# Performance work log

Hardware: AMD Instinct MI355X
Metric: run time of the kernel (lower is better)

The kernel has to match this reference:

```python
import jax, jax.numpy as jnp
import numpy as np
import math

BATCH, SEQ, D_MODEL, D_STATE = 8, 512, 2048, 16
DT_MIN, DT_MAX, DT_FLOOR, DT_SCALE = 0.001, 0.1, 1e-4, 1.0


def setup_inputs() -> dict:
    key = jax.random.key(0)
    k1, k2, k3, k4, k5 = jax.random.split(key, 5)
    x = jax.random.normal(k1, (BATCH, SEQ, D_MODEL), dtype=jnp.float32)
    # A_log = -exp(randn / sqrt(d_state))  (so A = exp(A_log) in (0,1))
    A_log = -jnp.exp(jax.random.normal(k2, (D_MODEL, D_STATE), dtype=jnp.float32) / math.sqrt(D_STATE))
    B = jax.random.normal(k3, (D_MODEL, D_STATE), dtype=jnp.float32) / math.sqrt(D_STATE)
    C = jax.random.normal(k4, (D_MODEL, D_STATE), dtype=jnp.float32) / math.sqrt(D_STATE)
    log_dt = jax.random.uniform(k5, (D_MODEL,), dtype=jnp.float32) * (math.log(DT_MAX) - math.log(DT_MIN)) + math.log(DT_MIN)
    log_dt = jnp.maximum(log_dt, jnp.float32(math.log(DT_FLOOR)))
    return {"x": x, "A_log": A_log, "B": B, "C": C, "log_dt": log_dt}


def reference(x, A_log, B, C, log_dt):
    # delta=None path: dt is per-channel, time-invariant -> dA, dB are [D, N]
    dt = jnp.exp(log_dt) * DT_SCALE                      # [D]
    A = jnp.exp(A_log)                                   # [D, N]
    dA = jnp.exp(dt[:, None] * A)                        # [D, N]  (matches torch einsum 'bld,dn->bldn' squeezed)
    dB = dt[:, None] * B                                 # [D, N]
    batch = x.shape[0]
    h0 = jnp.zeros((batch, D_MODEL, D_STATE), dtype=x.dtype)

    def step(h, xt):
        # xt: [B, D]
        h = dA * h + dB * xt[:, :, None]                 # [B, D, N]
        y = jnp.einsum('bdn,dn->bd', h, C)               # [B, D]
        return h, y

    _, ys = jax.lax.scan(step, h0, jnp.swapaxes(x, 0, 1))  # ys: [L, B, D]
    return jnp.swapaxes(ys, 0, 1)                          # [B, L, D]
```

## Files before the change

kernel.cpp:

```cpp
#include <hip/hip_runtime.h>
#include <math.h>


#define SSM_BATCH 8
#define SSM_SEQ 512
#define SSM_D 2048
#define SSM_N 16
#define NC 16
#define CL 32
#define DPB 64

typedef float float4v __attribute__((ext_vector_type(4)));

static __device__ inline float4v fma4(float4v a, float4v b, float4v c) {
    return (float4v){fmaf(a.x, b.x, c.x), fmaf(a.y, b.y, c.y),
                     fmaf(a.z, b.z, c.z), fmaf(a.w, b.w, c.w)};
}
static __device__ inline float4v exp4(float4v v) {
    return (float4v){expf(v.x), expf(v.y), expf(v.z), expf(v.w)};
}

__global__ __launch_bounds__(1024, 4) void ssm_fused3(
    const float* __restrict__ x, const float* __restrict__ A_log,
    const float* __restrict__ Bm, const float* __restrict__ Cm,
    const float* __restrict__ log_dt, float* __restrict__ out)
{
    const int tid = threadIdx.x;
    const int dl  = tid & (DPB - 1);
    const int c   = tid >> 6;
    const int d   = blockIdx.x * DPB + dl;
    const int b   = blockIdx.y;

    __shared__ float4v S4[DPB * 4 * 17];

    const size_t xoff = ((size_t)b * SSM_SEQ + c * CL) * SSM_D + d;
    const float* xp = x + xoff;

    float xb[CL];
    #pragma unroll
    for (int t = 0; t < CL; ++t) xb[t] = xp[(size_t)t * SSM_D];

    const float dt = expf(log_dt[d]);
    float4v dA[4];
    #pragma unroll
    for (int j = 0; j < 4; ++j) {
        float4v al = *(const float4v*)(A_log + d * SSM_N + 4 * j);
        dA[j] = exp4(dt * exp4(al));
    }

    float4v u[4];
    #pragma unroll
    for (int j = 0; j < 4; ++j) u[j] = (float4v)0.f;
    #pragma unroll
    for (int t = 0; t < CL; ++t) {
        const float xv = xb[t];
        const float4v xs = {xv, xv, xv, xv};
        #pragma unroll
        for (int j = 0; j < 4; ++j) u[j] = fma4(dA[j], u[j], xs);
    }
    #pragma unroll
    for (int j = 0; j < 4; ++j) S4[(dl * 4 + j) * 17 + c] = u[j];
    __syncthreads();

    if (tid < DPB * 4) {
        const int cdl = tid >> 2, g = tid & 3;
        const int dd  = blockIdx.x * DPB + cdl;
        const float dt2 = expf(log_dt[dd]);
        float4v al = *(const float4v*)(A_log + dd * SSM_N + 4 * g);
        float4v dAL = exp4(((float)CL * dt2) * exp4(al));
        float4v H = (float4v)0.f;
        float4v* row = &S4[(cdl * 4 + g) * 17];
        #pragma unroll
        for (int cc = 0; cc < NC; ++cc) {
            float4v s = row[cc];
            row[cc] = H;
            H = fma4(dAL, H, s);
        }
    }
    __syncthreads();

    float4v dBC[4];
    #pragma unroll
    for (int j = 0; j < 4; ++j) {
        float4v bv = *(const float4v*)(Bm + d * SSM_N + 4 * j);
        float4v cv = *(const float4v*)(Cm + d * SSM_N + 4 * j);
        dBC[j] = (dt * bv) * cv;
        u[j] = S4[(dl * 4 + j) * 17 + c];
    }

    float* op = out + xoff;
    #pragma unroll
    for (int t = 0; t < CL; ++t) {
        const float xv = xb[t];
        const float4v xs = {xv, xv, xv, xv};
        #pragma unroll
        for (int j = 0; j < 4; ++j) u[j] = fma4(dA[j], u[j], xs);
        float4v p = dBC[0] * u[0];
        p = fma4(dBC[1], u[1], p);
        p = fma4(dBC[2], u[2], p);
        p = fma4(dBC[3], u[3], p);
        op[(size_t)t * SSM_D] = (p.x + p.y) + (p.z + p.w);
    }
}

extern "C" void kernel_launch(void* const* d_in, const int* in_sizes, int n_in,
                              void* d_out, int out_size, void* d_ws, size_t ws_size,
                              hipStream_t stream) {
    const float* x      = (const float*)d_in[0];
    const float* A_log  = (const float*)d_in[1];
    const float* B      = (const float*)d_in[2];
    const float* C      = (const float*)d_in[3];
    const float* log_dt = (const float*)d_in[4];
    float* out = (float*)d_out;

    dim3 grid(SSM_D / DPB, SSM_BATCH);
    ssm_fused3<<<grid, DPB * NC, 0, stream>>>(x, A_log, B, C, log_dt, out);
}
```

Measured before the change: 100.8 us.

## Replace block barriers with per-chunk shared-memory flags for chunk-carry scan

Drops the two __syncthreads around the cross-chunk carry scan. Each wavefront now publishes its chunk-local state to shared memory and raises a flag. The last chunk's wavefront runs the serial carry scan, handing each chunk its incoming state through a second set of flags. Waiting chunks spin with s_sleep, so early chunks can start their output pass without waiting for the whole block. This trades barrier cost for spin-wait latency and polling overhead, and it relies on all 16 wavefronts of the block being resident at once to avoid deadlock.

```diff
diff --git a/kernel.cpp b/kernel.cpp
--- a/kernel.cpp
+++ b/kernel.cpp
@@ -20,7 +20,7 @@
     return (float4v){expf(v.x), expf(v.y), expf(v.z), expf(v.w)};
 }
 
-__global__ __launch_bounds__(1024, 4) void ssm_fused3(
+__global__ __launch_bounds__(1024, 4) void ssm_fused4(
     const float* __restrict__ x, const float* __restrict__ A_log,
     const float* __restrict__ Bm, const float* __restrict__ Cm,
     const float* __restrict__ log_dt, float* __restrict__ out)
@@ -32,10 +32,14 @@
     const int b   = blockIdx.y;
 
     __shared__ float4v S4[DPB * 4 * 17];
+    __shared__ unsigned uflag[NC];
+    __shared__ unsigned cflag[NC];
+
+    if (tid < NC) { uflag[tid] = 0u; cflag[tid] = 0u; }
+    __syncthreads();
 
     const size_t xoff = ((size_t)b * SSM_SEQ + c * CL) * SSM_D + d;
     const float* xp = x + xoff;
-
     float xb[CL];
     #pragma unroll
     for (int t = 0; t < CL; ++t) xb[t] = xp[(size_t)t * SSM_D];
@@ -58,26 +62,14 @@
         #pragma unroll
         for (int j = 0; j < 4; ++j) u[j] = fma4(dA[j], u[j], xs);
     }
-    #pragma unroll
-    for (int j = 0; j < 4; ++j) S4[(dl * 4 + j) * 17 + c] = u[j];
-    __syncthreads();
 
-    if (tid < DPB * 4) {
-        const int cdl = tid >> 2, g = tid & 3;
-        const int dd  = blockIdx.x * DPB + cdl;
-        const float dt2 = expf(log_dt[dd]);
-        float4v al = *(const float4v*)(A_log + dd * SSM_N + 4 * g);
-        float4v dAL = exp4(((float)CL * dt2) * exp4(al));
-        float4v H = (float4v)0.f;
-        float4v* row = &S4[(cdl * 4 + g) * 17];
+    const int row = dl * 4;
+    if (c < NC - 1) {
         #pragma unroll
-        for (int cc = 0; cc < NC; ++cc) {
-            float4v s = row[cc];
-            row[cc] = H;
-            H = fma4(dAL, H, s);
-        }
+        for (int j = 0; j < 4; ++j) S4[(row + j) * 17 + c] = u[j];
+        __threadfence_block();
+        if (dl == 0) atomicExch(&uflag[c], 1u);
     }
-    __syncthreads();
 
     float4v dBC[4];
     #pragma unroll
@@ -85,7 +77,42 @@
         float4v bv = *(const float4v*)(Bm + d * SSM_N + 4 * j);
         float4v cv = *(const float4v*)(Cm + d * SSM_N + 4 * j);
         dBC[j] = (dt * bv) * cv;
-        u[j] = S4[(dl * 4 + j) * 17 + c];
+    }
+
+    if (c == NC - 1) {
+        float4v dAL[4];
+        #pragma unroll
+        for (int j = 0; j < 4; ++j) {
+            float4v al = *(const float4v*)(A_log + d * SSM_N + 4 * j);
+            dAL[j] = exp4(((float)CL * dt) * exp4(al));
+        }
+        float4v H[4];
+        #pragma unroll
+        for (int j = 0; j < 4; ++j) H[j] = (float4v)0.f;
+
+        for (int cc = 0; cc < NC - 1; ++cc) {
+            while (atomicAdd(&uflag[cc], 0u) == 0u) __builtin_amdgcn_s_sleep(1);
+            __threadfence_block();
+            float4v Ucc[4];
+            #pragma unroll
+            for (int j = 0; j < 4; ++j) Ucc[j] = S4[(row + j) * 17 + cc];
+            #pragma unroll
+            for (int j = 0; j < 4; ++j) S4[(row + j) * 17 + cc] = H[j];
+            __threadfence_block();
+            if (dl == 0) atomicExch(&cflag[cc], 1u);
+            #pragma unroll
+            for (int j = 0; j < 4; ++j) H[j] = fma4(dAL[j], H[j], Ucc[j]);
+        }
+        #pragma unroll
+        for (int j = 0; j < 4; ++j) u[j] = H[j];
+    } else if (c == 0) {
+        #pragma unroll
+        for (int j = 0; j < 4; ++j) u[j] = (float4v)0.f;
+    } else {
+        while (atomicAdd(&cflag[c], 0u) == 0u) __builtin_amdgcn_s_sleep(1);
+        __threadfence_block();
+        #pragma unroll
+        for (int j = 0; j < 4; ++j) u[j] = S4[(row + j) * 17 + c];
     }
 
     float* op = out + xoff;
@@ -114,5 +141,5 @@
     float* out = (float*)d_out;
 
     dim3 grid(SSM_D / DPB, SSM_BATCH);
-    ssm_fused3<<<grid, DPB * NC, 0, stream>>>(x, A_log, B, C, log_dt, out);
+    ssm_fused4<<<grid, DPB * NC, 0, stream>>>(x, A_log, B, C, log_dt, out);
 }
```

Measured after the change: 112.9 us. 1.12x slower.

## Split chunked scan into two kernels with LDS-staged coalesced x tiles

Applied to the files above, without the earlier changes.

Replaces the single fused kernel, which used per-block chunk-state exchange in LDS, with two launches. The first computes per-chunk end states into a workspace. The second reads x again, rebuilds the carry-in state by serially combining earlier chunk states from global memory, and writes outputs. Both kernels stage x through LDS with float4 coalesced row loads and write output the same way, replacing strided per-thread column accesses. This adds a second read of x, an extra launch, and workspace traffic that grows with chunk index.

```diff
diff --git a/kernel.cpp b/kernel.cpp
--- a/kernel.cpp
+++ b/kernel.cpp
@@ -6,9 +6,9 @@
 #define SSM_SEQ 512
 #define SSM_D 2048
 #define SSM_N 16
-#define NC 16
-#define CL 32
-#define DPB 64
+#define NCH 8
+#define CLEN 64
+#define DT 256
 
 typedef float float4v __attribute__((ext_vector_type(4)));
 
@@ -20,26 +20,24 @@
     return (float4v){expf(v.x), expf(v.y), expf(v.z), expf(v.w)};
 }
 
-__global__ __launch_bounds__(1024, 4) void ssm_fused3(
+__global__ __launch_bounds__(256, 2) void ssm_k1(
     const float* __restrict__ x, const float* __restrict__ A_log,
-    const float* __restrict__ Bm, const float* __restrict__ Cm,
-    const float* __restrict__ log_dt, float* __restrict__ out)
+    const float* __restrict__ log_dt, float* __restrict__ U)
 {
-    const int tid = threadIdx.x;
-    const int dl  = tid & (DPB - 1);
-    const int c   = tid >> 6;
-    const int d   = blockIdx.x * DPB + dl;
-    const int b   = blockIdx.y;
+    const int tid   = threadIdx.x;
+    const int dtile = blockIdx.x, c = blockIdx.y, b = blockIdx.z;
+    __shared__ float xs[CLEN * DT];
 
-    __shared__ float4v S4[DPB * 4 * 17];
+    const int trow = tid >> 6;
+    const int col4 = (tid & 63) * 4;
+    const float* gx = x + ((size_t)(b * SSM_SEQ + c * CLEN)) * SSM_D + dtile * DT;
 
-    const size_t xoff = ((size_t)b * SSM_SEQ + c * CL) * SSM_D + d;
-    const float* xp = x + xoff;
+    float4 stg[16];
+    #pragma unroll
+    for (int r = 0; r < 16; ++r)
+        stg[r] = *(const float4*)(gx + (size_t)(r * 4 + trow) * SSM_D + col4);
 
-    float xb[CL];
-    #pragma unroll
-    for (int t = 0; t < CL; ++t) xb[t] = xp[(size_t)t * SSM_D];
-
+    const int d = dtile * DT + tid;
     const float dt = expf(log_dt[d]);
     float4v dA[4];
     #pragma unroll
@@ -48,58 +46,103 @@
         dA[j] = exp4(dt * exp4(al));
     }
 
+    #pragma unroll
+    for (int r = 0; r < 16; ++r)
+        *(float4*)(&xs[(r * 4 + trow) * DT + col4]) = stg[r];
+    __syncthreads();
+
     float4v u[4];
     #pragma unroll
     for (int j = 0; j < 4; ++j) u[j] = (float4v)0.f;
+    #pragma unroll 8
+    for (int t = 0; t < CLEN; ++t) {
+        const float xv = xs[t * DT + tid];
+        const float4v xsv = {xv, xv, xv, xv};
+        #pragma unroll
+        for (int j = 0; j < 4; ++j) u[j] = fma4(dA[j], u[j], xsv);
+    }
+
+    float* up = U + (((size_t)c * SSM_BATCH + b) * SSM_D + d) * SSM_N;
     #pragma unroll
-    for (int t = 0; t < CL; ++t) {
-        const float xv = xb[t];
-        const float4v xs = {xv, xv, xv, xv};
+    for (int j = 0; j < 4; ++j) *(float4v*)(up + 4 * j) = u[j];
+}
+
+__global__ __launch_bounds__(256, 2) void ssm_k2(
+    const float* __restrict__ x, const float* __restrict__ A_log,
+    const float* __restrict__ Bm, const float* __restrict__ Cm,
+    const float* __restrict__ log_dt, const float* __restrict__ U,
+    float* __restrict__ out)
+{
+    const int tid   = threadIdx.x;
+    const int dtile = blockIdx.x, c = blockIdx.y, b = blockIdx.z;
+    __shared__ float xs[CLEN * DT];
+
+    const int trow = tid >> 6;
+    const int col4 = (tid & 63) * 4;
+    const size_t goff = ((size_t)(b * SSM_SEQ + c * CLEN)) * SSM_D + dtile * DT;
+    const float* gx = x + goff;
+
+    float4 stg[16];
+    #pragma unroll
+    for (int r = 0; r < 16; ++r)
+        stg[r] = *(const float4*)(gx + (size_t)(r * 4 + trow) * SSM_D + col4);
+
+    const int d = dtile * DT + tid;
+    const float dt = expf(log_dt[d]);
+    float4v dA[4], dBC[4];
+    #pragma unroll
+    for (int j = 0; j < 4; ++j) {
+        float4v al = *(const float4v*)(A_log + d * SSM_N + 4 * j);
+        float4v bv = *(const float4v*)(Bm + d * SSM_N + 4 * j);
+        float4v cv = *(const float4v*)(Cm + d * SSM_N + 4 * j);
+        dA[j]  = exp4(dt * exp4(al));
+        dBC[j] = (dt * bv) * cv;
+    }
+
+    #pragma unroll
+    for (int r = 0; r < 16; ++r)
+        *(float4*)(&xs[(r * 4 + trow) * DT + col4]) = stg[r];
+
+    float4v H[4];
+    #pragma unroll
+    for (int j = 0; j < 4; ++j) H[j] = (float4v)0.f;
+    if (c > 0) {
+        float4v dAL[4];
         #pragma unroll
-        for (int j = 0; j < 4; ++j) u[j] = fma4(dA[j], u[j], xs);
-    }
-    #pragma unroll
-    for (int j = 0; j < 4; ++j) S4[(dl * 4 + j) * 17 + c] = u[j];
-    __syncthreads();
-
-    if (tid < DPB * 4) {
-        const int cdl = tid >> 2, g = tid & 3;
-        const int dd  = blockIdx.x * DPB + cdl;
-        const float dt2 = expf(log_dt[dd]);
-        float4v al = *(const float4v*)(A_log + dd * SSM_N + 4 * g);
-        float4v dAL = exp4(((float)CL * dt2) * exp4(al));
-        float4v H = (float4v)0.f;
-        float4v* row = &S4[(cdl * 4 + g) * 17];
-        #pragma unroll
-        for (int cc = 0; cc < NC; ++cc) {
-            float4v s = row[cc];
-            row[cc] = H;
-            H = fma4(dAL, H, s);
+        for (int j = 0; j < 4; ++j) {
+            float4v al = *(const float4v*)(A_log + d * SSM_N + 4 * j);
+            dAL[j] = exp4(((float)CLEN * dt) * exp4(al));
+        }
+        for (int cc = 0; cc < c; ++cc) {
+            const float* up = U + (((size_t)cc * SSM_BATCH + b) * SSM_D + d) * SSM_N;
+            float4v Uc[4];
+            #pragma unroll
+            for (int j = 0; j < 4; ++j) Uc[j] = *(const float4v*)(up + 4 * j);
+            #pragma unroll
+            for (int j = 0; j < 4; ++j) H[j] = fma4(dAL[j], H[j], Uc[j]);
         }
     }
     __syncthreads();
 
-    float4v dBC[4];
+    #pragma unroll 8
+    for (int t = 0; t < CLEN; ++t) {
+        const float xv = xs[t * DT + tid];
+        const float4v xsv = {xv, xv, xv, xv};
+        #pragma unroll
+        for (int j = 0; j < 4; ++j) H[j] = fma4(dA[j], H[j], xsv);
+        float4v p = dBC[0] * H[0];
+        p = fma4(dBC[1], H[1], p);
+        p = fma4(dBC[2], H[2], p);
+        p = fma4(dBC[3], H[3], p);
+        xs[t * DT + tid] = (p.x + p.y) + (p.z + p.w);
+    }
+    __syncthreads();
+
+    float* gy = out + goff;
     #pragma unroll
-    for (int j = 0; j < 4; ++j) {
-        float4v bv = *(const float4v*)(Bm + d * SSM_N + 4 * j);
-        float4v cv = *(const float4v*)(Cm + d * SSM_N + 4 * j);
-        dBC[j] = (dt * bv) * cv;
-        u[j] = S4[(dl * 4 + j) * 17 + c];
-    }
-
-    float* op = out + xoff;
-    #pragma unroll
-    for (int t = 0; t < CL; ++t) {
-        const float xv = xb[t];
-        const float4v xs = {xv, xv, xv, xv};
-        #pragma unroll
-        for (int j = 0; j < 4; ++j) u[j] = fma4(dA[j], u[j], xs);
-        float4v p = dBC[0] * u[0];
-        p = fma4(dBC[1], u[1], p);
-        p = fma4(dBC[2], u[2], p);
-        p = fma4(dBC[3], u[3], p);
-        op[(size_t)t * SSM_D] = (p.x + p.y) + (p.z + p.w);
+    for (int r = 0; r < 16; ++r) {
+        float4 v = *(const float4*)(&xs[(r * 4 + trow) * DT + col4]);
+        *(float4*)(gy + (size_t)(r * 4 + trow) * SSM_D + col4) = v;
     }
 }
 
@@ -112,7 +155,9 @@
     const float* C      = (const float*)d_in[3];
     const float* log_dt = (const float*)d_in[4];
     float* out = (float*)d_out;
+    float* U   = (float*)d_ws;
 
-    dim3 grid(SSM_D / DPB, SSM_BATCH);
-    ssm_fused3<<<grid, DPB * NC, 0, stream>>>(x, A_log, B, C, log_dt, out);
+    dim3 grid(SSM_D / DT, NCH, SSM_BATCH);
+    ssm_k1<<<grid, DT, 0, stream>>>(x, A_log, log_dt, U);
+    ssm_k2<<<grid, DT, 0, stream>>>(x, A_log, B, C, log_dt, U, out);
 }
```

New measurement: 106.5 us. 1.06x slower.
